# Optimization experiments

Measured on AMD Instinct MI355X. Metric: run time of the kernel, lower is better.

The kernel has to match this reference:

```python
import jax, jax.numpy as jnp
import numpy as np

N_NODES = 10000
N_EDGES = 100000
IN_CH = 384
PROJ = 768  # in_channels * projection_factor
N_BLOCKS = 4
OUT_CH = 128
LN_EPS = 1e-5


def _p(key, shape, fan_in):
    return jax.random.normal(key, shape, dtype=jnp.float32) * (1.0 / np.sqrt(fan_in))


def setup_inputs() -> dict:
    key = jax.random.key(0)
    ks = iter(jax.random.split(key, 64))
    x = jax.random.normal(next(ks), (N_NODES, IN_CH), dtype=jnp.float32)
    edge_index = jax.random.randint(next(ks), (2, N_EDGES), 0, N_NODES, dtype=jnp.int64)
    inp = {
        'x': x,
        'edge_index': edge_index,
        'proj_W': _p(next(ks), (PROJ, IN_CH), IN_CH),
        'proj_b': jnp.zeros((PROJ,), jnp.float32),
        'norm_w': jnp.ones((N_BLOCKS, PROJ), jnp.float32),
        'norm_b': jnp.zeros((N_BLOCKS, PROJ), jnp.float32),
        'g1_W': _p(next(ks), (N_BLOCKS, 4 * 192, PROJ), PROJ),
        'g1_as': _p(next(ks), (N_BLOCKS, 4, 192), 192),
        'g1_ad': _p(next(ks), (N_BLOCKS, 4, 192), 192),
        'g1_b': jnp.zeros((N_BLOCKS, 4 * 192), jnp.float32),
        'g2_W': _p(next(ks), (N_BLOCKS, 2 * 96, PROJ), PROJ),
        'g2_as': _p(next(ks), (N_BLOCKS, 2, 96), 96),
        'g2_ad': _p(next(ks), (N_BLOCKS, 2, 96), 96),
        'g2_b': jnp.zeros((N_BLOCKS, 2 * 96), jnp.float32),
        'uni_W': _p(next(ks), (N_BLOCKS, PROJ, 960), 960),
        'uni_b': jnp.zeros((N_BLOCKS, PROJ), jnp.float32),
        'fnorm_w': jnp.ones((PROJ,), jnp.float32),
        'fnorm_b': jnp.zeros((PROJ,), jnp.float32),
        'fg_W': _p(next(ks), (8 * OUT_CH, PROJ), PROJ),
        'fg_as': _p(next(ks), (8, OUT_CH), OUT_CH),
        'fg_ad': _p(next(ks), (8, OUT_CH), OUT_CH),
        'fg_b': jnp.zeros((OUT_CH,), jnp.float32),
    }
    return inp


def layer_norm(x, w, b):
    m = x.mean(-1, keepdims=True)
    v = ((x - m) ** 2).mean(-1, keepdims=True)
    return (x - m) / jnp.sqrt(v + LN_EPS) * w + b


def gat_conv(x, src, dst, W, a_src, a_dst, bias, heads, out_ch, concat):
    # PyG GATConv (eval mode, add_self_loops already applied in src/dst).
    n = x.shape[0]
    h = (x @ W.T).reshape(n, heads, out_ch)          # [N,H,C]
    al_s = jnp.einsum('nhc,hc->nh', h, a_src)        # [N,H]
    al_d = jnp.einsum('nhc,hc->nh', h, a_dst)
    e = jax.nn.leaky_relu(al_s[src] + al_d[dst], 0.2)  # [E,H]
    emax = jax.ops.segment_max(e, dst, num_segments=n)
    ee = jnp.exp(e - emax[dst])
    den = jax.ops.segment_sum(ee, dst, num_segments=n)
    alpha = ee / (den[dst] + 1e-16)                  # softmax over incoming edges
    out = jax.ops.segment_sum(h[src] * alpha[:, :, None], dst, num_segments=n)
    out = out.reshape(n, heads * out_ch) if concat else out.mean(axis=1)
    return out + bias


def reference(x, edge_index, proj_W, proj_b, norm_w, norm_b,
              g1_W, g1_as, g1_ad, g1_b, g2_W, g2_as, g2_ad, g2_b,
              uni_W, uni_b, fnorm_w, fnorm_b, fg_W, fg_as, fg_ad, fg_b):
    n = x.shape[0]
    loop = jnp.arange(n, dtype=edge_index.dtype)
    src = jnp.concatenate([edge_index[0], loop])  # add self loops (PyG default)
    dst = jnp.concatenate([edge_index[1], loop])

    h = jax.nn.elu(x @ proj_W.T + proj_b)
    for i in range(N_BLOCKS):
        res = h
        hn = layer_norm(h, norm_w[i], norm_b[i])
        o1 = gat_conv(hn, src, dst, g1_W[i], g1_as[i], g1_ad[i], g1_b[i], 4, 192, True)
        o2 = gat_conv(hn, src, dst, g2_W[i], g2_as[i], g2_ad[i], g2_b[i], 2, 96, True)
        cat = jax.nn.elu(jnp.concatenate([o1, o2], axis=-1))  # [N,960]
        h = jax.nn.elu(res + cat @ uni_W[i].T + uni_b[i])
    h = layer_norm(h, fnorm_w, fnorm_b)
    return gat_conv(h, src, dst, fg_W, fg_as, fg_ad, fg_b, 8, OUT_CH, False)
```

## Files before the change

kernel.cpp:

```cpp
#include <hip/hip_runtime.h>
#include <math.h>

#define N_NODES 10000
#define N_EDGES 100000
#define E_TOT   (N_EDGES + N_NODES)
#define PROJ    768
#define LN_EPS  1e-5f

typedef __attribute__((ext_vector_type(8))) short bf16x8;
typedef __attribute__((ext_vector_type(4))) short bf16x4;
typedef __attribute__((ext_vector_type(4))) float f32x4;

__device__ __forceinline__ float elu_f(float x){ return x > 0.f ? x : __expf(x) - 1.f; }
__device__ __forceinline__ float bf2f(unsigned short u){ return __uint_as_float(((unsigned int)u) << 16); }
__device__ __forceinline__ unsigned short f2bf(float f){
  unsigned int u = __float_as_uint(f);
  return (unsigned short)((u + 0x7FFFu + ((u >> 16) & 1u)) >> 16);
}

#define GLOAD16(gp, lp) __builtin_amdgcn_global_load_lds((const __attribute__((address_space(1))) void*)(gp), (__attribute__((address_space(3))) void*)(lp), 16, 0, 0)

__global__ void k_count(const int* __restrict__ ei, int* __restrict__ cnt){
  int e = blockIdx.x*blockDim.x + threadIdx.x;
  if (e >= E_TOT) return;
  int dst = (e < N_EDGES) ? ei[N_EDGES + e] : (e - N_EDGES);
  atomicAdd(&cnt[dst], 1);
}

__global__ void k_scan(const int* __restrict__ cnt, int* __restrict__ indptr){
  __shared__ int s[1024];
  __shared__ int s_running;
  int t = threadIdx.x;
  if (t == 0) s_running = 0;
  __syncthreads();
  for (int base = 0; base < N_NODES; base += 1024){
    int v = (base + t < N_NODES) ? cnt[base + t] : 0;
    s[t] = v; __syncthreads();
    for (int off = 1; off < 1024; off <<= 1){
      int add = (t >= off) ? s[t - off] : 0;
      __syncthreads();
      s[t] += add;
      __syncthreads();
    }
    int total = s[1023];
    int run = s_running;
    if (base + t < N_NODES) indptr[base + t] = run + s[t] - v;
    __syncthreads();
    if (t == 0) s_running = run + total;
    __syncthreads();
  }
  if (t == 0) indptr[N_NODES] = s_running;
}

__global__ void k_copy_int(const int* __restrict__ src, int* __restrict__ dst, int n){
  int i = blockIdx.x*blockDim.x + threadIdx.x;
  if (i < n) dst[i] = src[i];
}

__global__ void k_fill(const int* __restrict__ ei, int* __restrict__ pos,
                       int* __restrict__ csr_src, int* __restrict__ csr_dst){
  int e = blockIdx.x*blockDim.x + threadIdx.x;
  if (e >= E_TOT) return;
  int s, d;
  if (e < N_EDGES){ s = ei[e]; d = ei[N_EDGES + e]; }
  else            { s = d = e - N_EDGES; }
  int p = atomicAdd(&pos[d], 1);
  csr_src[p] = s;
  csr_dst[p] = d;
}

__global__ void k_f2bf_arr4(const float4* __restrict__ in, ushort4* __restrict__ out, int n4){
  int i = blockIdx.x*blockDim.x + threadIdx.x;
  if (i < n4){
    float4 v = in[i];
    ushort4 o;
    o.x = f2bf(v.x); o.y = f2bf(v.y); o.z = f2bf(v.z); o.w = f2bf(v.w);
    out[i] = o;
  }
}

__global__ void k_pack_l1l2(const float* __restrict__ g1, const float* __restrict__ g2,
                            unsigned short* __restrict__ dst){
  int i = blockIdx.x*blockDim.x + threadIdx.x;
  if (i >= 737280) return;
  int layer = i / 184320;
  int off4  = i - layer*184320;
  float4 v;
  if (off4 < 147456) v = *((const float4*)(g1 + (size_t)layer*589824) + off4);
  else               v = *((const float4*)(g2 + (size_t)layer*147456) + (off4 - 147456));
  ushort4 o;
  o.x = f2bf(v.x); o.y = f2bf(v.y); o.z = f2bf(v.z); o.w = f2bf(v.w);
  ((ushort4*)(dst + (size_t)layer*737280))[off4] = o;
}

__global__ void k_layernorm_bf(const unsigned short* __restrict__ x, const float* __restrict__ w,
                               const float* __restrict__ b, unsigned short* __restrict__ y){
  int n = blockIdx.x;
  int t = threadIdx.x;
  const unsigned short* xr = x + (size_t)n*PROJ;
  float v0=0.f, v1=0.f, v2=0.f, v3=0.f;
  if (t < 192){
    bf16x4 hv = *(const bf16x4*)(xr + t*4);
    v0 = bf2f((unsigned short)hv.x); v1 = bf2f((unsigned short)hv.y);
    v2 = bf2f((unsigned short)hv.z); v3 = bf2f((unsigned short)hv.w);
  }
  float s  = v0+v1+v2+v3;
  float s2 = v0*v0 + v1*v1 + v2*v2 + v3*v3;
  #pragma unroll
  for (int off = 32; off; off >>= 1){ s += __shfl_down(s, off); s2 += __shfl_down(s2, off); }
  __shared__ float rs[4], rs2[4];
  __shared__ float s_mean, s_rstd;
  int wid = t >> 6, lane = t & 63;
  if (lane == 0){ rs[wid] = s; rs2[wid] = s2; }
  __syncthreads();
  if (t == 0){
    float S  = rs[0]+rs[1]+rs[2]+rs[3];
    float S2 = rs2[0]+rs2[1]+rs2[2]+rs2[3];
    float m  = S * (1.f/768.f);
    float var = S2 * (1.f/768.f) - m*m;
    s_mean = m; s_rstd = rsqrtf(var + LN_EPS);
  }
  __syncthreads();
  if (t < 192){
    float m = s_mean, r = s_rstd;
    float4 wv = *(const float4*)&w[t*4];
    float4 bv = *(const float4*)&b[t*4];
    ushort4 o;
    o.x = f2bf((v0-m)*r*wv.x + bv.x);
    o.y = f2bf((v1-m)*r*wv.y + bv.y);
    o.z = f2bf((v2-m)*r*wv.z + bv.z);
    o.w = f2bf((v3-m)*r*wv.w + bv.w);
    *(ushort4*)(y + (size_t)n*PROJ + t*4) = o;
  }
}

template<int EPI>
__global__ __launch_bounds__(256, 3)
void k_gemm_mfma(const unsigned short* __restrict__ A, int lda,
                 const unsigned short* __restrict__ W,
                 unsigned short* __restrict__ C, int ldc,
                 int M, int N, int K,
                 const float* __restrict__ bias,
                 const unsigned short* __restrict__ res, int ldres, int NBN){
  __shared__ unsigned short As[2][128*64];
  __shared__ unsigned short Bs[2][64*64];
  const int tid = threadIdx.x;
  const int lane = tid & 63, wid = tid >> 6;
  const int wm = wid >> 1, wn = wid & 1;

  const int nwg = gridDim.x;
  const int q = nwg >> 3, r = nwg & 7;
  const int xcd = blockIdx.x & 7, o = blockIdx.x >> 3;
  const int swz = (xcd < r ? xcd*(q+1) : r*(q+1) + (xcd - r)*q) + o;
  const int bm = (swz / NBN) * 128;
  const int bn = (swz % NBN) * 64;

  const int srow = tid >> 3;
  const int sc16 = (tid & 7) ^ (srow & 7);
  size_t ga[4], gb[2];
  #pragma unroll
  for (int p = 0; p < 4; p++)
    ga[p] = (size_t)min(bm + p*32 + srow, M-1)*lda + sc16*8;
  #pragma unroll
  for (int p = 0; p < 2; p++)
    gb[p] = (size_t)min(bn + p*32 + srow, N-1)*K + sc16*8;
  const int ldst = tid*8;

  f32x4 acc[4][2];
  #pragma unroll
  for (int i=0;i<4;i++)
    #pragma unroll
    for (int j=0;j<2;j++) acc[i][j] = (f32x4){0.f,0.f,0.f,0.f};

  const int rA = wm*64 + (lane & 15);
  const int rB = wn*32 + (lane & 15);

  const int NT = K >> 6;
  int cur = 0;
  #pragma unroll
  for (int p = 0; p < 4; p++) GLOAD16(A + ga[p], &As[0][p*2048 + ldst]);
  #pragma unroll
  for (int p = 0; p < 2; p++) GLOAD16(W + gb[p], &Bs[0][p*2048 + ldst]);

  for (int t = 0; t < NT; ++t){
    if (t + 1 < NT){
      const int k0 = (t+1) << 6;
      #pragma unroll
      for (int p = 0; p < 4; p++) GLOAD16(A + ga[p] + k0, &As[cur^1][p*2048 + ldst]);
      #pragma unroll
      for (int p = 0; p < 2; p++) GLOAD16(W + gb[p] + k0, &Bs[cur^1][p*2048 + ldst]);
      asm volatile("s_waitcnt vmcnt(6)" ::: "memory");
    } else {
      asm volatile("s_waitcnt vmcnt(0)" ::: "memory");
    }
    __builtin_amdgcn_sched_barrier(0);
    __builtin_amdgcn_s_barrier();
    __builtin_amdgcn_sched_barrier(0);

    #pragma unroll
    for (int kk = 0; kk < 2; kk++){
      bf16x8 af[4], bfr[2];
      const int cA = (((kk<<2) | (lane>>4)) ^ (lane&7)) * 8;
      #pragma unroll
      for (int mi = 0; mi < 4; mi++)
        af[mi] = *(const bf16x8*)&As[cur][(rA + mi*16)*64 + cA];
      #pragma unroll
      for (int ni = 0; ni < 2; ni++)
        bfr[ni] = *(const bf16x8*)&Bs[cur][(rB + ni*16)*64 + cA];
      #pragma unroll
      for (int mi = 0; mi < 4; mi++)
        #pragma unroll
        for (int ni = 0; ni < 2; ni++)
          acc[mi][ni] = __builtin_amdgcn_mfma_f32_16x16x32_bf16(af[mi], bfr[ni], acc[mi][ni], 0,0,0);
    }
    asm volatile("s_waitcnt lgkmcnt(0)" ::: "memory");
    __builtin_amdgcn_sched_barrier(0);
    __builtin_amdgcn_s_barrier();
    __builtin_amdgcn_sched_barrier(0);
    cur ^= 1;
  }

  const int mrow0 = bm + wm*64 + ((lane>>4)<<2);
  const int ncol0 = bn + wn*32 + (lane & 15);
  #pragma unroll
  for (int mi=0; mi<4; mi++){
    #pragma unroll
    for (int rr=0; rr<4; rr++){
      int m = mrow0 + mi*16 + rr;
      if (m >= M) continue;
      #pragma unroll
      for (int ni=0; ni<2; ni++){
        int n = ncol0 + ni*16;
        float v = acc[mi][ni][rr];
        if (EPI == 1){
          v = elu_f(v + bias[n]);
        } else if (EPI == 2){
          v = elu_f(v + bias[n] + bf2f(res[(size_t)m*ldres + n]));
        }
        C[(size_t)m*ldc + n] = f2bf(v);
      }
    }
  }
}

__global__ void k_attn_coef6(const unsigned short* __restrict__ hlin,
                             const float* __restrict__ as1, const float* __restrict__ ad1,
                             const float* __restrict__ as2, const float* __restrict__ ad2,
                             float* __restrict__ als, float* __restrict__ ald){
  int n = blockIdx.x;
  int wid = threadIdx.x >> 6, lane = threadIdx.x & 63;
  int C    = wid < 4 ? 192 : 96;
  int base = wid < 4 ? wid*192 : 768 + (wid-4)*96;
  const float* as_ = wid < 4 ? as1 + wid*192 : as2 + (wid-4)*96;
  const float* ad_ = wid < 4 ? ad1 + wid*192 : ad2 + (wid-4)*96;
  float ss = 0.f, sd = 0.f;
  if (lane*4 < C){
    bf16x4 hv = *(const bf16x4*)(hlin + (size_t)n*960 + base + lane*4);
    float4 a1 = *(const float4*)&as_[lane*4];
    float4 a2 = *(const float4*)&ad_[lane*4];
    float h0 = bf2f((unsigned short)hv.x), h1 = bf2f((unsigned short)hv.y);
    float h2 = bf2f((unsigned short)hv.z), h3 = bf2f((unsigned short)hv.w);
    ss = h0*a1.x + h1*a1.y + h2*a1.z + h3*a1.w;
    sd = h0*a2.x + h1*a2.y + h2*a2.z + h3*a2.w;
  }
  #pragma unroll
  for (int off = 32; off; off >>= 1){ ss += __shfl_down(ss, off); sd += __shfl_down(sd, off); }
  if (lane == 0){ als[n*6 + wid] = ss; ald[n*6 + wid] = sd; }
}

__global__ void k_attn_coef8(const unsigned short* __restrict__ hlin,
                             const float* __restrict__ a_src, const float* __restrict__ a_dst,
                             float* __restrict__ als, float* __restrict__ ald){
  int n = blockIdx.x;
  int wid = threadIdx.x >> 6, lane = threadIdx.x & 63;
  float ss = 0.f, sd = 0.f;
  if (lane < 32){
    bf16x4 hv = *(const bf16x4*)(hlin + (size_t)n*1024 + wid*128 + lane*4);
    float4 a1 = *(const float4*)&a_src[wid*128 + lane*4];
    float4 a2 = *(const float4*)&a_dst[wid*128 + lane*4];
    float h0 = bf2f((unsigned short)hv.x), h1 = bf2f((unsigned short)hv.y);
    float h2 = bf2f((unsigned short)hv.z), h3 = bf2f((unsigned short)hv.w);
    ss = h0*a1.x + h1*a1.y + h2*a1.z + h3*a1.w;
    sd = h0*a2.x + h1*a2.y + h2*a2.z + h3*a2.w;
  }
  #pragma unroll
  for (int off = 32; off; off >>= 1){ ss += __shfl_down(ss, off); sd += __shfl_down(sd, off); }
  if (lane == 0){ als[n*8 + wid] = ss; ald[n*8 + wid] = sd; }
}

template<int HT>
__global__ void k_attn_stats(const float* __restrict__ als, const float* __restrict__ ald,
                             const int* __restrict__ indptr, const int* __restrict__ csr_src,
                             float* __restrict__ mo, float* __restrict__ dio){
  int n = blockIdx.x;
  int wv = threadIdx.x >> 6, lane = threadIdx.x & 63;
  int beg = indptr[n], end = indptr[n+1];
  float aldv = ald[n*HT + wv];
  float m = -1e30f, d = 0.f;
  for (int e = beg + lane; e < end; e += 64){
    int s = csr_src[e];
    float v = als[s*HT + wv] + aldv;
    v = v > 0.f ? v : 0.2f*v;
    if (v > m){ d *= __expf(m - v); m = v; }
    d += __expf(v - m);
  }
  #pragma unroll
  for (int off = 1; off < 64; off <<= 1){
    float mo_ = __shfl_xor(m, off);
    float dd  = __shfl_xor(d, off);
    float mn  = fmaxf(m, mo_);
    d = d*__expf(m - mn) + dd*__expf(mo_ - mn);
    m = mn;
  }
  if (lane == 0){ mo[n*HT + wv] = m; dio[n*HT + wv] = 1.f/(d + 1e-16f); }
}

template<int HT>
__global__ void k_attn_alpha(const float* __restrict__ als, const float* __restrict__ ald,
                             const int* __restrict__ csr_src, const int* __restrict__ csr_dst,
                             const float* __restrict__ m, const float* __restrict__ dinv,
                             float* __restrict__ alpha){
  int i = blockIdx.x*blockDim.x + threadIdx.x;
  if (i >= E_TOT*HT) return;
  int e = i / HT, h = i - e*HT;
  int s = csr_src[e], d = csr_dst[e];
  float v = als[s*HT + h] + ald[d*HT + h];
  v = v > 0.f ? v : 0.2f*v;
  alpha[i] = __expf(v - m[d*HT + h]) * dinv[d*HT + h];
}

template<int MODE>
__global__ __launch_bounds__(256)
void k_attn_agg2(const unsigned short* __restrict__ hlin, int ldh,
                 const float* __restrict__ alpha,
                 const int* __restrict__ indptr, const int* __restrict__ csr_src,
                 const float* __restrict__ b1, const float* __restrict__ b2,
                 void* __restrict__ outv, int ldo){
  constexpr int TOT = MODE ? 1024 : 960;
  constexpr int HT  = MODE ? 8 : 6;
  constexpr int CHUNKS = TOT/4;
  constexpr int CPL = (CHUNKS + 63)/64;
  int n = blockIdx.x;
  int tid = threadIdx.x;
  int wv = tid >> 6, lane = tid & 63;
  int beg = indptr[n], end = indptr[n+1];

  __shared__ float s_red[4][TOT];

  int hof[CPL];
  #pragma unroll
  for (int p = 0; p < CPL; p++){
    int ch4 = (lane + p*64)*4;
    hof[p] = MODE ? (ch4 >> 7) : (ch4 < 768 ? ch4/192 : 4 + (ch4-768)/96);
  }

  f32x4 acc[CPL];
  #pragma unroll
  for (int p = 0; p < CPL; p++) acc[p] = (f32x4){0.f,0.f,0.f,0.f};

  for (int e = beg + wv; e < end; e += 4){
    int s = csr_src[e];
    const bf16x4* hr = (const bf16x4*)(hlin + (size_t)s*ldh);
    const float* ae = alpha + (size_t)e*HT;
    #pragma unroll
    for (int p = 0; p < CPL; p++){
      int ch = lane + p*64;
      if (CHUNKS % 64 == 0 || ch < CHUNKS){
        float al = ae[hof[p]];
        bf16x4 hv = hr[ch];
        acc[p].x += bf2f((unsigned short)hv.x)*al;
        acc[p].y += bf2f((unsigned short)hv.y)*al;
        acc[p].z += bf2f((unsigned short)hv.z)*al;
        acc[p].w += bf2f((unsigned short)hv.w)*al;
      }
    }
  }

  #pragma unroll
  for (int p = 0; p < CPL; p++){
    int ch = lane + p*64;
    if (CHUNKS % 64 == 0 || ch < CHUNKS)
      *(f32x4*)&s_red[wv][ch*4] = acc[p];
  }
  __syncthreads();

  if (MODE == 0){
    unsigned short* out = (unsigned short*)outv;
    #pragma unroll
    for (int qq = 0; qq < 4; qq++){
      int idx = tid + qq*256;
      if (idx < TOT){
        float bb = idx < 768 ? b1[idx] : b2[idx - 768];
        float v = s_red[0][idx] + s_red[1][idx] + s_red[2][idx] + s_red[3][idx] + bb;
        out[(size_t)n*ldo + idx] = f2bf(elu_f(v));
      }
    }
  } else {
    float* out = (float*)outv;
    if (tid < 128){
      float v = 0.f;
      #pragma unroll
      for (int h = 0; h < 8; h++){
        int idx = h*128 + tid;
        v += s_red[0][idx] + s_red[1][idx] + s_red[2][idx] + s_red[3][idx];
      }
      out[(size_t)n*ldo + tid] = v*0.125f + b1[tid];
    }
  }
}

extern "C" void kernel_launch(void* const* d_in, const int* in_sizes, int n_in,
                              void* d_out, int out_size, void* d_ws, size_t ws_size,
                              hipStream_t stream){
  const float* x      = (const float*)d_in[0];
  const int*   ei     = (const int*)  d_in[1];
  const float* proj_W = (const float*)d_in[2];
  const float* proj_b = (const float*)d_in[3];
  const float* norm_w = (const float*)d_in[4];
  const float* norm_b = (const float*)d_in[5];
  const float* g1_W   = (const float*)d_in[6];
  const float* g1_as  = (const float*)d_in[7];
  const float* g1_ad  = (const float*)d_in[8];
  const float* g1_b   = (const float*)d_in[9];
  const float* g2_W   = (const float*)d_in[10];
  const float* g2_as  = (const float*)d_in[11];
  const float* g2_ad  = (const float*)d_in[12];
  const float* g2_b   = (const float*)d_in[13];
  const float* uni_W  = (const float*)d_in[14];
  const float* uni_b  = (const float*)d_in[15];
  const float* fnorm_w= (const float*)d_in[16];
  const float* fnorm_b= (const float*)d_in[17];
  const float* fg_W   = (const float*)d_in[18];
  const float* fg_as  = (const float*)d_in[19];
  const float* fg_ad  = (const float*)d_in[20];
  const float* fg_b   = (const float*)d_in[21];

  float* w = (float*)d_ws;
  unsigned short* h  = (unsigned short*)w; w += 3840000;
  unsigned short* h2 = (unsigned short*)w; w += 3840000;
  unsigned short* linbuf = (unsigned short*)w; w += 5120000;
  unsigned short* hnb  = (unsigned short*)w; w += 3840000;
  unsigned short* catb = (unsigned short*)w; w += 4800000;
  unsigned short* wb   = (unsigned short*)w; w += 3489792;
  float* als   = w; w += 80000;
  float* ald   = w; w += 80000;
  float* mbuf  = w; w += 80000;
  float* dibuf = w; w += 80000;
  float* alphab= w; w += 880000;
  int* iw = (int*)w;
  int* cnt     = iw; iw += 10016;
  int* indptr  = iw; iw += 10016;
  int* pos     = iw; iw += 10016;
  int* csr_src = iw; iw += 110016;
  int* csr_dst = iw; iw += 110016;

  unsigned short* wb_proj = wb;
  unsigned short* wb_l12  = wb_proj + 294912;
  unsigned short* wb_uni  = wb_l12 + 2949120;
  unsigned short* wb_fg   = wb_uni + 2949120;

  hipMemsetAsync(cnt, 0, N_NODES*sizeof(int), stream);
  k_count<<<(E_TOT+255)/256, 256, 0, stream>>>(ei, cnt);
  k_scan<<<1, 1024, 0, stream>>>(cnt, indptr);
  k_copy_int<<<(N_NODES+255)/256, 256, 0, stream>>>(indptr, pos, N_NODES);
  k_fill<<<(E_TOT+255)/256, 256, 0, stream>>>(ei, pos, csr_src, csr_dst);

  k_f2bf_arr4<<<(960000+255)/256, 256, 0, stream>>>((const float4*)x, (ushort4*)hnb, 960000);
  k_f2bf_arr4<<<(73728+255)/256,  256, 0, stream>>>((const float4*)proj_W, (ushort4*)wb_proj, 73728);
  k_pack_l1l2<<<(737280+255)/256, 256, 0, stream>>>(g1_W, g2_W, wb_l12);
  k_f2bf_arr4<<<(737280+255)/256, 256, 0, stream>>>((const float4*)uni_W, (ushort4*)wb_uni, 737280);
  k_f2bf_arr4<<<(196608+255)/256, 256, 0, stream>>>((const float4*)fg_W, (ushort4*)wb_fg, 196608);

  dim3 blk(256);

  k_gemm_mfma<1><<<dim3(79*12), blk, 0, stream>>>(hnb, 384, wb_proj, h, 768, N_NODES, 768, 384, proj_b, nullptr, 0, 12);

  unsigned short* cur = h;
  unsigned short* oth = h2;
  for (int i = 0; i < 4; i++){
    k_layernorm_bf<<<N_NODES, 256, 0, stream>>>(cur, norm_w + i*768, norm_b + i*768, hnb);
    k_gemm_mfma<0><<<dim3(79*15), blk, 0, stream>>>(hnb, 768, wb_l12 + (size_t)i*737280, linbuf, 960, N_NODES, 960, 768, nullptr, nullptr, 0, 15);
    k_attn_coef6<<<N_NODES, 384, 0, stream>>>(linbuf, g1_as + i*768, g1_ad + i*768, g2_as + i*192, g2_ad + i*192, als, ald);
    k_attn_stats<6><<<N_NODES, 384, 0, stream>>>(als, ald, indptr, csr_src, mbuf, dibuf);
    k_attn_alpha<6><<<(E_TOT*6+255)/256, 256, 0, stream>>>(als, ald, csr_src, csr_dst, mbuf, dibuf, alphab);
    k_attn_agg2<0><<<N_NODES, 256, 0, stream>>>(linbuf, 960, alphab, indptr, csr_src, g1_b + i*768, g2_b + i*192, catb, 960);
    k_gemm_mfma<2><<<dim3(79*12), blk, 0, stream>>>(catb, 960, wb_uni + (size_t)i*737280, oth, 768, N_NODES, 768, 960, uni_b + i*768, cur, 768, 12);
    unsigned short* t = cur; cur = oth; oth = t;
  }

  k_layernorm_bf<<<N_NODES, 256, 0, stream>>>(cur, fnorm_w, fnorm_b, hnb);
  k_gemm_mfma<0><<<dim3(79*16), blk, 0, stream>>>(hnb, 768, wb_fg, linbuf, 1024, N_NODES, 1024, 768, nullptr, nullptr, 0, 16);
  k_attn_coef8<<<N_NODES, 512, 0, stream>>>(linbuf, fg_as, fg_ad, als, ald);
  k_attn_stats<8><<<N_NODES, 512, 0, stream>>>(als, ald, indptr, csr_src, mbuf, dibuf);
  k_attn_alpha<8><<<(E_TOT*8+255)/256, 256, 0, stream>>>(als, ald, csr_src, csr_dst, mbuf, dibuf, alphab);
  k_attn_agg2<1><<<N_NODES, 256, 0, stream>>>(linbuf, 1024, alphab, indptr, csr_src, fg_b, nullptr, d_out, 128);
}
```

Measured before the change: 762.7 us.

## Shrink GEMM K-tile to 32 for higher occupancy, widen aggregation loads to 16B

The MFMA GEMM now stages 32-wide K slices instead of 64, which halves shared memory per block, raises the launch-bounds occupancy target from 3 to 8 blocks, and changes the LDS swizzle and fill pattern to match. The attention aggregation kernel loads 8 bf16 values (16 bytes) per lane instead of 4, so each lane holds two accumulators and fewer lanes are active per edge. The aim is to hide GEMM memory latency with more resident waves and to cut load instructions in the gather. The cost is twice as many barrier and wait steps per unit of K in the GEMM, and a tighter register budget that could cause spills.

```diff
diff --git a/kernel.cpp b/kernel.cpp
--- a/kernel.cpp
+++ b/kernel.cpp
@@ -135,15 +135,15 @@
 }
 
 template<int EPI>
-__global__ __launch_bounds__(256, 3)
+__global__ __launch_bounds__(256, 8)
 void k_gemm_mfma(const unsigned short* __restrict__ A, int lda,
                  const unsigned short* __restrict__ W,
                  unsigned short* __restrict__ C, int ldc,
                  int M, int N, int K,
                  const float* __restrict__ bias,
                  const unsigned short* __restrict__ res, int ldres, int NBN){
-  __shared__ unsigned short As[2][128*64];
-  __shared__ unsigned short Bs[2][64*64];
+  __shared__ unsigned short As[2][128*32];
+  __shared__ unsigned short Bs[2][64*32];
   const int tid = threadIdx.x;
   const int lane = tid & 63, wid = tid >> 6;
   const int wm = wid >> 1, wn = wid & 1;
@@ -155,15 +155,11 @@
   const int bm = (swz / NBN) * 128;
   const int bn = (swz % NBN) * 64;
 
-  const int srow = tid >> 3;
-  const int sc16 = (tid & 7) ^ (srow & 7);
-  size_t ga[4], gb[2];
-  #pragma unroll
-  for (int p = 0; p < 4; p++)
-    ga[p] = (size_t)min(bm + p*32 + srow, M-1)*lda + sc16*8;
-  #pragma unroll
-  for (int p = 0; p < 2; p++)
-    gb[p] = (size_t)min(bn + p*32 + srow, N-1)*K + sc16*8;
+  const int srow = tid >> 2;
+  const int sc   = (tid & 3) ^ ((tid >> 3) & 3);
+  size_t ga0 = (size_t)min(bm + srow,      M-1)*lda + sc*8;
+  size_t ga1 = (size_t)min(bm + 64 + srow, M-1)*lda + sc*8;
+  size_t gb0 = (size_t)min(bn + srow,      N-1)*K   + sc*8;
   const int ldst = tid*8;
 
   f32x4 acc[4][2];
@@ -174,22 +170,21 @@
 
   const int rA = wm*64 + (lane & 15);
   const int rB = wn*32 + (lane & 15);
-
-  const int NT = K >> 6;
+  const int cu = (((lane >> 4)) ^ (((lane & 15) >> 1) & 3)) * 8;
+
+  const int NT = K >> 5;
   int cur = 0;
-  #pragma unroll
-  for (int p = 0; p < 4; p++) GLOAD16(A + ga[p], &As[0][p*2048 + ldst]);
-  #pragma unroll
-  for (int p = 0; p < 2; p++) GLOAD16(W + gb[p], &Bs[0][p*2048 + ldst]);
+  GLOAD16(A + ga0, &As[0][ldst]);
+  GLOAD16(A + ga1, &As[0][2048 + ldst]);
+  GLOAD16(W + gb0, &Bs[0][ldst]);
 
   for (int t = 0; t < NT; ++t){
     if (t + 1 < NT){
-      const int k0 = (t+1) << 6;
-      #pragma unroll
-      for (int p = 0; p < 4; p++) GLOAD16(A + ga[p] + k0, &As[cur^1][p*2048 + ldst]);
-      #pragma unroll
-      for (int p = 0; p < 2; p++) GLOAD16(W + gb[p] + k0, &Bs[cur^1][p*2048 + ldst]);
-      asm volatile("s_waitcnt vmcnt(6)" ::: "memory");
+      const int k0 = (t+1) << 5;
+      GLOAD16(A + ga0 + k0, &As[cur^1][ldst]);
+      GLOAD16(A + ga1 + k0, &As[cur^1][2048 + ldst]);
+      GLOAD16(W + gb0 + k0, &Bs[cur^1][ldst]);
+      asm volatile("s_waitcnt vmcnt(3)" ::: "memory");
     } else {
       asm volatile("s_waitcnt vmcnt(0)" ::: "memory");
     }
@@ -197,22 +192,19 @@
     __builtin_amdgcn_s_barrier();
     __builtin_amdgcn_sched_barrier(0);
 
-    #pragma unroll
-    for (int kk = 0; kk < 2; kk++){
-      bf16x8 af[4], bfr[2];
-      const int cA = (((kk<<2) | (lane>>4)) ^ (lane&7)) * 8;
-      #pragma unroll
-      for (int mi = 0; mi < 4; mi++)
-        af[mi] = *(const bf16x8*)&As[cur][(rA + mi*16)*64 + cA];
+    bf16x8 af[4], bfr[2];
+    #pragma unroll
+    for (int mi = 0; mi < 4; mi++)
+      af[mi] = *(const bf16x8*)&As[cur][(rA + mi*16)*32 + cu];
+    #pragma unroll
+    for (int ni = 0; ni < 2; ni++)
+      bfr[ni] = *(const bf16x8*)&Bs[cur][(rB + ni*16)*32 + cu];
+    #pragma unroll
+    for (int mi = 0; mi < 4; mi++)
       #pragma unroll
       for (int ni = 0; ni < 2; ni++)
-        bfr[ni] = *(const bf16x8*)&Bs[cur][(rB + ni*16)*64 + cA];
-      #pragma unroll
-      for (int mi = 0; mi < 4; mi++)
-        #pragma unroll
-        for (int ni = 0; ni < 2; ni++)
-          acc[mi][ni] = __builtin_amdgcn_mfma_f32_16x16x32_bf16(af[mi], bfr[ni], acc[mi][ni], 0,0,0);
-    }
+        acc[mi][ni] = __builtin_amdgcn_mfma_f32_16x16x32_bf16(af[mi], bfr[ni], acc[mi][ni], 0,0,0);
+
     asm volatile("s_waitcnt lgkmcnt(0)" ::: "memory");
     __builtin_amdgcn_sched_barrier(0);
     __builtin_amdgcn_s_barrier();
@@ -338,8 +330,8 @@
                  void* __restrict__ outv, int ldo){
   constexpr int TOT = MODE ? 1024 : 960;
   constexpr int HT  = MODE ? 8 : 6;
-  constexpr int CHUNKS = TOT/4;
-  constexpr int CPL = (CHUNKS + 63)/64;
+  constexpr int CH8 = TOT/8;
+  constexpr int CPL = (CH8 + 63)/64;
   int n = blockIdx.x;
   int tid = threadIdx.x;
   int wv = tid >> 6, lane = tid & 63;
@@ -350,28 +342,32 @@
   int hof[CPL];
   #pragma unroll
   for (int p = 0; p < CPL; p++){
-    int ch4 = (lane + p*64)*4;
-    hof[p] = MODE ? (ch4 >> 7) : (ch4 < 768 ? ch4/192 : 4 + (ch4-768)/96);
-  }
-
-  f32x4 acc[CPL];
-  #pragma unroll
-  for (int p = 0; p < CPL; p++) acc[p] = (f32x4){0.f,0.f,0.f,0.f};
+    int idx = (lane + p*64)*8;
+    hof[p] = MODE ? (idx >> 7) : (idx < 768 ? idx/192 : 4 + (idx-768)/96);
+  }
+
+  f32x4 accA[CPL], accB[CPL];
+  #pragma unroll
+  for (int p = 0; p < CPL; p++){ accA[p] = (f32x4){0,0,0,0}; accB[p] = (f32x4){0,0,0,0}; }
 
   for (int e = beg + wv; e < end; e += 4){
     int s = csr_src[e];
-    const bf16x4* hr = (const bf16x4*)(hlin + (size_t)s*ldh);
+    const bf16x8* hr = (const bf16x8*)(hlin + (size_t)s*ldh);
     const float* ae = alpha + (size_t)e*HT;
     #pragma unroll
     for (int p = 0; p < CPL; p++){
       int ch = lane + p*64;
-      if (CHUNKS % 64 == 0 || ch < CHUNKS){
+      if (CH8 % 64 == 0 || ch < CH8){
         float al = ae[hof[p]];
-        bf16x4 hv = hr[ch];
-        acc[p].x += bf2f((unsigned short)hv.x)*al;
-        acc[p].y += bf2f((unsigned short)hv.y)*al;
-        acc[p].z += bf2f((unsigned short)hv.z)*al;
-        acc[p].w += bf2f((unsigned short)hv.w)*al;
+        bf16x8 hv = hr[ch];
+        accA[p].x += bf2f((unsigned short)hv[0])*al;
+        accA[p].y += bf2f((unsigned short)hv[1])*al;
+        accA[p].z += bf2f((unsigned short)hv[2])*al;
+        accA[p].w += bf2f((unsigned short)hv[3])*al;
+        accB[p].x += bf2f((unsigned short)hv[4])*al;
+        accB[p].y += bf2f((unsigned short)hv[5])*al;
+        accB[p].z += bf2f((unsigned short)hv[6])*al;
+        accB[p].w += bf2f((unsigned short)hv[7])*al;
       }
     }
   }
@@ -379,8 +375,10 @@
   #pragma unroll
   for (int p = 0; p < CPL; p++){
     int ch = lane + p*64;
-    if (CHUNKS % 64 == 0 || ch < CHUNKS)
-      *(f32x4*)&s_red[wv][ch*4] = acc[p];
+    if (CH8 % 64 == 0 || ch < CH8){
+      *(f32x4*)&s_red[wv][ch*8]     = accA[p];
+      *(f32x4*)&s_red[wv][ch*8 + 4] = accB[p];
+    }
   }
   __syncthreads();
 
```

New measurement: 765.2 us. No clear change (+0.3%).
